# Performance work log

Measured on AMD Instinct MI355X. Metric: run time of the kernel, lower is better.

Reference implementation:

```python
import jax, jax.numpy as jnp
import numpy as np

B, C, H, W = 8, 256, 64, 64
NUM_HEADS = 8
HEAD_DIM = C // NUM_HEADS  # 32
KSIZE = 3
DILATIONS = [1, 2, 3, 4]
SCALE = HEAD_DIM ** -0.5


def _unfold(x, k, dil):
    # x: (B, d, H, W) -> (B, d, k*k, H, W), matching torch nn.Unfold with
    # padding = dil*(k-1)//2 and channel-major patch ordering.
    p = dil * (k - 1) // 2
    xp = jnp.pad(x, ((0, 0), (0, 0), (p, p), (p, p)))
    h, w = x.shape[2], x.shape[3]
    patches = [xp[:, :, i * dil:i * dil + h, j * dil:j * dil + w]
               for i in range(k) for j in range(k)]
    return jnp.stack(patches, axis=2)


def setup_inputs() -> dict:
    key = jax.random.key(0)
    k1, k2, k3, k4, k5 = jax.random.split(key, 5)
    x = jax.random.normal(k1, (B, C, H, W), dtype=jnp.float32)
    w_qkv = jax.random.normal(k2, (3 * C, C), dtype=jnp.float32) * 0.02
    b_qkv = jnp.zeros((3 * C,), dtype=jnp.float32)
    w_proj = jax.random.normal(k3, (C, C), dtype=jnp.float32) * 0.02
    b_proj = jnp.zeros((C,), dtype=jnp.float32)
    return {"x": x, "w_qkv": w_qkv, "b_qkv": b_qkv,
            "w_proj": w_proj, "b_proj": b_proj}


def reference(x, w_qkv, b_qkv, w_proj, b_proj):
    b, c, h, w = x.shape
    # 1x1 conv qkv projection
    qkv = jnp.einsum('bchw,oc->bohw', x, w_qkv) + b_qkv[None, :, None, None]
    qkv = qkv.reshape(b, 3, NUM_HEADS, HEAD_DIM, h, w)
    outs = []
    for hd in range(NUM_HEADS):  # small fixed loop; heads structurally distinct (dilation)
        dil = DILATIONS[hd % len(DILATIONS)]
        q = qkv[:, 0, hd]   # (B, d, H, W)
        k_ = qkv[:, 1, hd]
        v = qkv[:, 2, hd]
        kk = _unfold(k_, KSIZE, dil)  # (B, d, K2, H, W)
        vv = _unfold(v, KSIZE, dil)
        attn = jax.nn.softmax(
            jnp.einsum('bdhw,bdKhw->bKhw', q, kk) * SCALE, axis=1)
        outs.append(jnp.einsum('bKhw,bdKhw->bdhw', attn, vv))
    # torch.stack(dim=1).reshape(B,C,H,W) => head-major channel concat
    out = jnp.concatenate(outs, axis=1)  # (B, C, H, W)
    out = jnp.einsum('bchw,oc->bohw', out, w_proj) + b_proj[None, :, None, None]
    return out
```

## Files before the change

kernel.cpp:

```cpp
#include <hip/hip_runtime.h>
#include <cstdint>

typedef unsigned short ushortT;
typedef __attribute__((ext_vector_type(8))) short short8;
typedef __attribute__((ext_vector_type(8))) unsigned short ushort8v;
typedef __attribute__((ext_vector_type(4))) float float4v;

#define ATT_SCALE 0.17677669529663687f

__device__ inline float bf2f(unsigned short u) {
    union { unsigned int i; float f; } x; x.i = ((unsigned int)u) << 16; return x.f;
}
__device__ inline unsigned short f2bf(float f) {
    union { float f; unsigned int i; } x; x.f = f;
    unsigned int i = x.i;
    i += 0x7fffu + ((i >> 16) & 1u);
    return (unsigned short)(i >> 16);
}

__device__ inline void gld_lds16(const ushortT* g, ushortT* l) {
    __builtin_amdgcn_global_load_lds((const __attribute__((address_space(1))) void*)g,
                                     (__attribute__((address_space(3))) void*)l, 16, 0, 0);
}

__global__ __launch_bounds__(256) void convert_params(const float* __restrict__ w_qkv,
                                                      const float* __restrict__ w_proj,
                                                      const float* __restrict__ b_qkv,
                                                      const float* __restrict__ b_proj,
                                                      ushortT* __restrict__ wqkvB,
                                                      ushortT* __restrict__ wprojB,
                                                      float* __restrict__ bqF,
                                                      float* __restrict__ bpF) {
    int i = blockIdx.x * 256 + threadIdx.x;
    if (i < 196608) {
        wqkvB[i] = f2bf(w_qkv[i]);
    } else if (i < 262144) {
        wprojB[i - 196608] = f2bf(w_proj[i - 196608]);
    } else if (i < 262912) {
        bqF[i - 262144] = b_qkv[i - 262144];
    } else if (i < 263168) {
        bpF[i - 262912] = b_proj[i - 262912];
    }
}

__global__ __launch_bounds__(256) void transpose_cp(const float* __restrict__ x,
                                                    ushortT* __restrict__ xT) {
    __shared__ __align__(16) ushortT tile[64][65];
    const int b  = blockIdx.z;
    const int c0 = blockIdx.x * 64;
    const int p0 = blockIdx.y * 64;
    const int t  = threadIdx.x;

    const float* xb = x + (size_t)b * 256 * 4096;
#pragma unroll
    for (int it = 0; it < 4; it++) {
        int id  = t + it * 256;
        int row = id >> 4;
        int c4  = (id & 15) * 4;
        float4 v = *(const float4*)(xb + (size_t)(c0 + row) * 4096 + p0 + c4);
        tile[row][c4 + 0] = f2bf(v.x);
        tile[row][c4 + 1] = f2bf(v.y);
        tile[row][c4 + 2] = f2bf(v.z);
        tile[row][c4 + 3] = f2bf(v.w);
    }
    __syncthreads();
    ushortT* xTb = xT + (size_t)b * 4096 * 256;
#pragma unroll
    for (int it = 0; it < 2; it++) {
        int id   = t + it * 256;
        int prow = id >> 3;
        int cc   = (id & 7) * 8;
        ushort8v v;
#pragma unroll
        for (int j = 0; j < 8; j++) v[j] = tile[cc + j][prow];
        *(ushort8v*)(xTb + (size_t)(p0 + prow) * 256 + c0 + cc) = v;
    }
}

__global__ __launch_bounds__(256) void gemm_bt(const ushortT* __restrict__ A,
                                               const ushortT* __restrict__ Bt, long long sBb,
                                               int ldb, int bHeadMajor,
                                               void* __restrict__ D, long long sDb,
                                               int ldd, int dHeadMajor, int outF32,
                                               const float* __restrict__ bias, int biasAlongM,
                                               int K, int swizzleMode) {
    __shared__ __align__(16) ushortT pool[16384];

    int mIdx, nIdx, bz;
    {
        int id = blockIdx.x;
        int r  = id & 7;
        int j  = id >> 3;
        if (swizzleMode == 0) {
            mIdx = r * 32 + j / 6;
            nIdx = j % 6;
            bz   = 0;
        } else {
            int p = r * 32 + (j >> 1);
            bz   = p >> 5;
            nIdx = p & 31;
            mIdx = j & 1;
        }
    }
    const int n0 = nIdx * 128;
    const int m0 = mIdx * 128;
    Bt += (size_t)bz * sBb;

    const int t    = threadIdx.x;
    const int wv   = t >> 6;
    const int lane = t & 63;
    const int lm   = lane & 15;
    const int quad = lane >> 4;
    const int wm   = wv & 1;
    const int wn   = wv >> 1;

    ushortT* Als = pool;
    ushortT* Bls = pool + 4096;

    float4v acc[4][4];
#pragma unroll
    for (int i = 0; i < 4; i++)
#pragma unroll
        for (int j = 0; j < 4; j++) { float4v z = {0.f, 0.f, 0.f, 0.f}; acc[i][j] = z; }

    const int nkt = K >> 5;
    for (int kt = 0; kt < nkt; ++kt) {
        __syncthreads();
#pragma unroll
        for (int j = 0; j < 2; j++) {
            int cid = wv * 128 + j * 64 + lane;
            int row = cid >> 2;
            int c8  = cid & 3;
            int gc  = c8 ^ ((row >> 1) & 3);
            const ushortT* ga = A + (size_t)(m0 + row) * K + kt * 32 + gc * 8;
            const ushortT* gb = bHeadMajor
                ? Bt + ((size_t)kt * 32768 + (n0 + row)) * 32 + gc * 8
                : Bt + (size_t)(n0 + row) * ldb + kt * 32 + gc * 8;
            gld_lds16(ga, Als + (size_t)(wv * 128 + j * 64) * 8);
            gld_lds16(gb, Bls + (size_t)(wv * 128 + j * 64) * 8);
        }
        asm volatile("s_waitcnt vmcnt(0)" ::: "memory");
        __syncthreads();

        short8 af[4], bfr[4];
#pragma unroll
        for (int i = 0; i < 4; i++) {
            int r = wm * 64 + i * 16 + lm;
            int slot = quad ^ ((r >> 1) & 3);
            af[i] = *(const short8*)&Als[r * 32 + slot * 8];
        }
#pragma unroll
        for (int j = 0; j < 4; j++) {
            int r = wn * 64 + j * 16 + lm;
            int slot = quad ^ ((r >> 1) & 3);
            bfr[j] = *(const short8*)&Bls[r * 32 + slot * 8];
        }
#pragma unroll
        for (int i = 0; i < 4; i++)
#pragma unroll
            for (int j = 0; j < 4; j++)
                acc[i][j] = __builtin_amdgcn_mfma_f32_16x16x32_bf16(af[i], bfr[j], acc[i][j], 0, 0, 0);
    }

    if (dHeadMajor) {
        __syncthreads();
#pragma unroll
        for (int i = 0; i < 4; i++) {
#pragma unroll
            for (int j = 0; j < 4; j++) {
                int c = wn * 64 + j * 16 + lm;
#pragma unroll
                for (int rg = 0; rg < 4; rg++) {
                    int r = wm * 64 + i * 16 + quad * 4 + rg;
                    float v = acc[i][j][rg] + bias[biasAlongM ? (m0 + r) : (n0 + c)];
                    int chunk = (c >> 3) ^ (r & 7);
                    pool[r * 128 + chunk * 8 + (c & 7)] = f2bf(v);
                }
            }
        }
        __syncthreads();
        ushortT* Dh = (ushortT*)D + (size_t)bz * sDb;
#pragma unroll
        for (int g = 0; g < 4; g++) {
            ushortT* base = Dh + ((size_t)((n0 >> 5) + g) * 32768 + m0) * 32;
#pragma unroll
            for (int it = 0; it < 2; it++) {
                int id = it * 256 + t;
                int r  = id >> 2;
                int cb = id & 3;
                int pch = (g * 4 + cb) ^ (r & 7);
                ushort8v v = *(const ushort8v*)&pool[r * 128 + pch * 8];
                *(ushort8v*)(base + r * 32 + cb * 8) = v;
            }
        }
    } else {
        float*   Df = (float*)D   + (size_t)bz * sDb;
        ushortT* Dh = (ushortT*)D + (size_t)bz * sDb;
#pragma unroll
        for (int i = 0; i < 4; i++) {
            int r0 = m0 + wm * 64 + i * 16 + quad * 4;
#pragma unroll
            for (int j = 0; j < 4; j++) {
                int c = n0 + wn * 64 + j * 16 + lm;
#pragma unroll
                for (int rg = 0; rg < 4; rg++) {
                    int r = r0 + rg;
                    float v = acc[i][j][rg] + bias[biasAlongM ? r : c];
                    if (outF32) Df[(size_t)r * ldd + c] = v;
                    else        Dh[(size_t)r * ldd + c] = f2bf(v);
                }
            }
        }
    }
}

__global__ __launch_bounds__(256) void attn_k(ushortT* qkv) {
    const int gt   = blockIdx.x * 256 + threadIdx.x;
    const int lane = gt & 63;
    const int wid  = gt >> 6;
    const int hd   = wid >> 9;
    const int rowI = wid & 511;
    const int b    = rowI >> 6;
    const int h    = rowI & 63;
    const int w    = lane;
    const int dil  = (hd & 3) + 1;
    const int bp   = b * 4096 + h * 64 + w;

    ushortT*       qp    = qkv + ((size_t)hd * 32768 + bp) * 32;
    const ushortT* kbase = qkv + ((size_t)(8  + hd) * 32768 + (size_t)b * 4096) * 32;
    const ushortT* vbase = qkv + ((size_t)(16 + hd) * 32768 + (size_t)b * 4096) * 32;

    float q[32];
#pragma unroll
    for (int c = 0; c < 4; c++) {
        ushort8v v = *(const ushort8v*)(qp + c * 8);
#pragma unroll
        for (int j = 0; j < 8; j++) q[c * 8 + j] = bf2f(v[j]);
    }

    float lgt[9];
    int   nb[9];
    unsigned vmask = 0;
#pragma unroll
    for (int ii = 0; ii < 3; ii++) {
#pragma unroll
        for (int jj = 0; jj < 3; jj++) {
            int idx = ii * 3 + jj;
            int hh = h + (ii - 1) * dil;
            int ww = w + (jj - 1) * dil;
            bool ok = ((unsigned)hh < 64u) && ((unsigned)ww < 64u);
            int pp = (hh << 6) + ww;
            nb[idx] = pp;
            float l = 0.f;
            if (ok) {
                vmask |= (1u << idx);
                const ushortT* kp = kbase + (size_t)pp * 32;
#pragma unroll
                for (int c = 0; c < 4; c++) {
                    ushort8v v = *(const ushort8v*)(kp + c * 8);
#pragma unroll
                    for (int j = 0; j < 8; j++) l += q[c * 8 + j] * bf2f(v[j]);
                }
                l *= ATT_SCALE;
            }
            lgt[idx] = l;
        }
    }

    float mx = lgt[0];
#pragma unroll
    for (int i = 1; i < 9; i++) mx = fmaxf(mx, lgt[i]);
    float e[9], s = 0.f;
#pragma unroll
    for (int i = 0; i < 9; i++) { e[i] = __expf(lgt[i] - mx); s += e[i]; }
    const float inv = 1.f / s;

    float acc[32];
#pragma unroll
    for (int d = 0; d < 32; d++) acc[d] = 0.f;
#pragma unroll
    for (int idx = 0; idx < 9; idx++) {
        if ((vmask >> idx) & 1u) {
            float pj = e[idx] * inv;
            const ushortT* vp = vbase + (size_t)nb[idx] * 32;
#pragma unroll
            for (int c = 0; c < 4; c++) {
                ushort8v v = *(const ushort8v*)(vp + c * 8);
#pragma unroll
                for (int j = 0; j < 8; j++) acc[c * 8 + j] += pj * bf2f(v[j]);
            }
        }
    }

#pragma unroll
    for (int c = 0; c < 4; c++) {
        ushort8v v;
#pragma unroll
        for (int j = 0; j < 8; j++) v[j] = f2bf(acc[c * 8 + j]);
        *(ushort8v*)(qp + c * 8) = v;
    }
}

extern "C" void kernel_launch(void* const* d_in, const int* in_sizes, int n_in,
                              void* d_out, int out_size, void* d_ws, size_t ws_size,
                              hipStream_t stream) {
    const float* x      = (const float*)d_in[0];
    const float* w_qkv  = (const float*)d_in[1];
    const float* b_qkv  = (const float*)d_in[2];
    const float* w_proj = (const float*)d_in[3];
    const float* b_proj = (const float*)d_in[4];

    char* ws = (char*)d_ws;
    float*   bqF    = (float*)(ws + 256);
    float*   bpF    = (float*)(ws + 3328);
    ushortT* wqkvB  = (ushortT*)(ws + 4352);
    ushortT* wprojB = (ushortT*)(ws + 397568);
    ushortT* qkv    = (ushortT*)(ws + 528640);
    ushortT* xT     = (ushortT*)d_out;

    convert_params<<<1028, 256, 0, stream>>>(w_qkv, w_proj, b_qkv, b_proj,
                                             wqkvB, wprojB, bqF, bpF);

    transpose_cp<<<dim3(4, 64, 8), 256, 0, stream>>>(x, xT);

    gemm_bt<<<dim3(1536), 256, 0, stream>>>(xT, wqkvB, 0, 256, 0,
                                            qkv, 0, 0, 1, 0,
                                            bqF, 0, 256, 0);

    attn_k<<<dim3(1024), 256, 0, stream>>>(qkv);

    gemm_bt<<<dim3(512), 256, 0, stream>>>(wprojB, qkv, (long long)4096 * 32, 0, 1,
                                           d_out, (long long)256 * 4096, 4096, 0, 1,
                                           bpF, 1, 256, 1);
}
```

Before: 178.3 us.

## Fuse param conversion into transpose kernel and stage fp32 GEMM output through LDS

Folds the weight/bias conversion work into the transpose kernel's first 1028 blocks, removing one kernel launch. Separately, the fp32 output path of the projection GEMM now writes accumulators into a rotated LDS buffer in two passes and then emits coalesced float4 row stores, replacing scattered scalar global stores. The staging adds extra barriers and LDS traffic in the epilogue, and the fused transpose blocks carry some extra work.

Measured after the change: 173.0 us. 1.03x faster.

```diff
diff --git a/kernel.cpp b/kernel.cpp
--- a/kernel.cpp
+++ b/kernel.cpp
@@ -23,33 +23,37 @@
                                      (__attribute__((address_space(3))) void*)l, 16, 0, 0);
 }
 
-__global__ __launch_bounds__(256) void convert_params(const float* __restrict__ w_qkv,
-                                                      const float* __restrict__ w_proj,
-                                                      const float* __restrict__ b_qkv,
-                                                      const float* __restrict__ b_proj,
-                                                      ushortT* __restrict__ wqkvB,
-                                                      ushortT* __restrict__ wprojB,
-                                                      float* __restrict__ bqF,
-                                                      float* __restrict__ bpF) {
-    int i = blockIdx.x * 256 + threadIdx.x;
-    if (i < 196608) {
-        wqkvB[i] = f2bf(w_qkv[i]);
-    } else if (i < 262144) {
-        wprojB[i - 196608] = f2bf(w_proj[i - 196608]);
-    } else if (i < 262912) {
-        bqF[i - 262144] = b_qkv[i - 262144];
-    } else if (i < 263168) {
-        bpF[i - 262912] = b_proj[i - 262912];
-    }
-}
-
 __global__ __launch_bounds__(256) void transpose_cp(const float* __restrict__ x,
-                                                    ushortT* __restrict__ xT) {
+                                                    ushortT* __restrict__ xT,
+                                                    const float* __restrict__ w_qkv,
+                                                    const float* __restrict__ w_proj,
+                                                    const float* __restrict__ b_qkv,
+                                                    const float* __restrict__ b_proj,
+                                                    ushortT* __restrict__ wqkvB,
+                                                    ushortT* __restrict__ wprojB,
+                                                    float* __restrict__ bqF,
+                                                    float* __restrict__ bpF) {
     __shared__ __align__(16) ushortT tile[64][65];
     const int b  = blockIdx.z;
     const int c0 = blockIdx.x * 64;
     const int p0 = blockIdx.y * 64;
     const int t  = threadIdx.x;
+
+    {
+        int flat = blockIdx.x + 4 * blockIdx.y + 256 * blockIdx.z;
+        if (flat < 1028) {
+            int i = flat * 256 + t;
+            if (i < 196608) {
+                wqkvB[i] = f2bf(w_qkv[i]);
+            } else if (i < 262144) {
+                wprojB[i - 196608] = f2bf(w_proj[i - 196608]);
+            } else if (i < 262912) {
+                bqF[i - 262144] = b_qkv[i - 262144];
+            } else if (i < 263168) {
+                bpF[i - 262912] = b_proj[i - 262912];
+            }
+        }
+    }
 
     const float* xb = x + (size_t)b * 256 * 4096;
 #pragma unroll
@@ -193,8 +197,41 @@
                 *(ushort8v*)(base + r * 32 + cb * 8) = v;
             }
         }
+    } else if (outF32) {
+        float* poolF = (float*)pool;
+        float* Df = (float*)D + (size_t)bz * sDb;
+#pragma unroll
+        for (int pass = 0; pass < 2; pass++) {
+            __syncthreads();
+            if (wm == pass) {
+#pragma unroll
+                for (int i = 0; i < 4; i++) {
+#pragma unroll
+                    for (int j = 0; j < 4; j++) {
+                        int c = wn * 64 + j * 16 + lm;
+#pragma unroll
+                        for (int rg = 0; rg < 4; rg++) {
+                            int r64 = i * 16 + quad * 4 + rg;
+                            float v = acc[i][j][rg] +
+                                      bias[biasAlongM ? (m0 + pass * 64 + r64) : (n0 + c)];
+                            int phys = (c + 4 * r64) & 127;
+                            poolF[r64 * 128 + phys] = v;
+                        }
+                    }
+                }
+            }
+            __syncthreads();
+#pragma unroll
+            for (int it = 0; it < 8; it++) {
+                int id  = it * 256 + t;
+                int r64 = id >> 5;
+                int c   = (id & 31) * 4;
+                int phys = (c + 4 * r64) & 127;
+                float4 v = *(const float4*)&poolF[r64 * 128 + phys];
+                *(float4*)&Df[(size_t)(m0 + pass * 64 + r64) * ldd + n0 + c] = v;
+            }
+        }
     } else {
-        float*   Df = (float*)D   + (size_t)bz * sDb;
         ushortT* Dh = (ushortT*)D + (size_t)bz * sDb;
 #pragma unroll
         for (int i = 0; i < 4; i++) {
@@ -206,8 +243,7 @@
                 for (int rg = 0; rg < 4; rg++) {
                     int r = r0 + rg;
                     float v = acc[i][j][rg] + bias[biasAlongM ? r : c];
-                    if (outF32) Df[(size_t)r * ldd + c] = v;
-                    else        Dh[(size_t)r * ldd + c] = f2bf(v);
+                    Dh[(size_t)r * ldd + c] = f2bf(v);
                 }
             }
         }
@@ -318,10 +354,8 @@
     ushortT* qkv    = (ushortT*)(ws + 528640);
     ushortT* xT     = (ushortT*)d_out;
 
-    convert_params<<<1028, 256, 0, stream>>>(w_qkv, w_proj, b_qkv, b_proj,
-                                             wqkvB, wprojB, bqF, bpF);
-
-    transpose_cp<<<dim3(4, 64, 8), 256, 0, stream>>>(x, xT);
+    transpose_cp<<<dim3(4, 64, 8), 256, 0, stream>>>(x, xT, w_qkv, w_proj, b_qkv, b_proj,
+                                                     wqkvB, wprojB, bqF, bpF);
 
     gemm_bt<<<dim3(1536), 256, 0, stream>>>(xT, wqkvB, 0, 256, 0,
                                             qkv, 0, 0, 1, 0,
```
